# Kernel optimization log

Measured on AMD Instinct MI355X. Metric: run time of the kernel, lower is better.

Reference implementation:

```python
import jax, jax.numpy as jnp
import numpy as np

EPS = 1e-08


def setup_inputs() -> dict:
    key = jax.random.key(0)
    B, C, T = 4, 512, 32000
    x = jax.random.normal(key, (B, C, T), dtype=jnp.float32)
    weight = jnp.ones((C,), dtype=jnp.float32)
    bias = jnp.zeros((C,), dtype=jnp.float32)
    return {"x": x, "weight": weight, "bias": bias}


def reference(x, weight, bias):
    # Cumulative LayerNorm over (C, 0..t) for each time step t, 3D input (B, C, T).
    # Note: sum_C(cumsum_T(x)) == cumsum_T(sum_C(x)); reduce channels first (cheaper, same math).
    B, C, T = x.shape
    step = jnp.arange(1, T + 1, dtype=x.dtype)            # (T,)
    count = (step * C)[None, None, :]                     # (1,1,T)
    cum_sum = jnp.cumsum(x.sum(axis=1, keepdims=True), axis=-1)          # (B,1,T)
    cum_sum_sq = jnp.cumsum((x * x).sum(axis=1, keepdims=True), axis=-1)  # (B,1,T)
    cum_mean = cum_sum / count
    cum_var = jnp.maximum(cum_sum_sq / count - cum_mean * cum_mean, 0.0)
    y = (x - cum_mean) / jnp.sqrt(cum_var + EPS)
    return y * weight[None, :, None] + bias[None, :, None]
```

## Files before the change

### kernel.cpp

```cpp
#include <hip/hip_runtime.h>
#include <math.h>

#define EPS 1e-8

constexpr int CSPLIT = 4;
constexpr int CH = 1024;

__global__ __launch_bounds__(256) void clnorm_colsum(
    const float* __restrict__ x, float* __restrict__ psum,
    float* __restrict__ psumsq, int B, int C, int T) {
  int t = blockIdx.x * 256 + threadIdx.x;
  if (t >= T) return;
  int b = blockIdx.y;
  int s = blockIdx.z;
  int cPer = C / CSPLIT;
  const float* xp = x + ((size_t)b * C + (size_t)s * cPer) * (size_t)T + t;
  float sum = 0.f, sq = 0.f;
#pragma unroll 8
  for (int c = 0; c < cPer; ++c) {
    float v = xp[(size_t)c * T];
    sum += v;
    sq = fmaf(v, v, sq);
  }
  size_t o = ((size_t)s * B + b) * (size_t)T + t;
  psum[o] = sum;
  psumsq[o] = sq;
}

__global__ __launch_bounds__(256) void clnorm_chunktot(
    const float* __restrict__ psum, const float* __restrict__ psumsq,
    double* __restrict__ chunkTot, int B, int T, int nCh) {
  int ch = blockIdx.x;
  int b = blockIdx.y;
  int tid = threadIdx.x;
  int base = ch * CH;

  double ls = 0.0, lq = 0.0;
#pragma unroll
  for (int j = 0; j < CH / 256; ++j) {
    int t = base + tid + j * 256;
    if (t < T) {
      float s = 0.f, q = 0.f;
#pragma unroll
      for (int k = 0; k < CSPLIT; ++k) {
        size_t o = ((size_t)k * B + b) * (size_t)T + t;
        s += psum[o];
        q += psumsq[o];
      }
      ls += (double)s;
      lq += (double)q;
    }
  }
  __shared__ double sh_s[256];
  __shared__ double sh_q[256];
  sh_s[tid] = ls;
  sh_q[tid] = lq;
  __syncthreads();
  for (int off = 128; off > 0; off >>= 1) {
    if (tid < off) {
      sh_s[tid] += sh_s[tid + off];
      sh_q[tid] += sh_q[tid + off];
    }
    __syncthreads();
  }
  if (tid == 0) {
    chunkTot[((size_t)b * nCh + ch) * 2 + 0] = sh_s[0];
    chunkTot[((size_t)b * nCh + ch) * 2 + 1] = sh_q[0];
  }
}

__global__ __launch_bounds__(256) void clnorm_scanemit(
    const float* __restrict__ psum, const float* __restrict__ psumsq,
    const double* __restrict__ chunkTot, float* __restrict__ mean,
    float* __restrict__ rstd, int B, int C, int T, int nCh) {
  int ch = blockIdx.x;
  int b = blockIdx.y;
  int tid = threadIdx.x;
  int base = ch * CH;

  __shared__ double sv_s[CH];
  __shared__ double sv_q[CH];
  __shared__ double tp_s[256];
  __shared__ double tp_q[256];
  __shared__ double off_sq[2];

  if (tid == 0) {
    double os = 0.0, oq = 0.0;
    for (int c0 = 0; c0 < ch; ++c0) {
      os += chunkTot[((size_t)b * nCh + c0) * 2 + 0];
      oq += chunkTot[((size_t)b * nCh + c0) * 2 + 1];
    }
    off_sq[0] = os;
    off_sq[1] = oq;
  }

#pragma unroll
  for (int j = 0; j < CH / 256; ++j) {
    int idx = tid + j * 256;
    int t = base + idx;
    float s = 0.f, q = 0.f;
    if (t < T) {
#pragma unroll
      for (int k = 0; k < CSPLIT; ++k) {
        size_t o = ((size_t)k * B + b) * (size_t)T + t;
        s += psum[o];
        q += psumsq[o];
      }
    }
    sv_s[idx] = (double)s;
    sv_q[idx] = (double)q;
  }
  __syncthreads();

  const int E = CH / 256;
  double ts = 0.0, tq = 0.0;
#pragma unroll
  for (int j = 0; j < E; ++j) {
    ts += sv_s[tid * E + j];
    tq += sv_q[tid * E + j];
  }
  tp_s[tid] = ts;
  tp_q[tid] = tq;
  __syncthreads();
  for (int off = 1; off < 256; off <<= 1) {
    double vs = (tid >= off) ? tp_s[tid - off] : 0.0;
    double vq = (tid >= off) ? tp_q[tid - off] : 0.0;
    __syncthreads();
    tp_s[tid] += vs;
    tp_q[tid] += vq;
    __syncthreads();
  }
  double run_s = off_sq[0] + tp_s[tid] - ts;
  double run_q = off_sq[1] + tp_q[tid] - tq;

  int idx0 = tid * E;
  int t0 = base + idx0;
  float m_out[E], r_out[E];
#pragma unroll
  for (int j = 0; j < E; ++j) {
    run_s += sv_s[idx0 + j];
    run_q += sv_q[idx0 + j];
    double cnt = (double)(t0 + j + 1) * (double)C;
    double m = run_s / cnt;
    double var = run_q / cnt - m * m;
    if (var < 0.0) var = 0.0;
    m_out[j] = (float)m;
    r_out[j] = (float)(1.0 / sqrt(var + EPS));
  }
  size_t mo = (size_t)b * T + t0;
  if (t0 + E <= T) {
    *(float4*)(mean + mo) = make_float4(m_out[0], m_out[1], m_out[2], m_out[3]);
    *(float4*)(rstd + mo) = make_float4(r_out[0], r_out[1], r_out[2], r_out[3]);
  } else {
    for (int j = 0; j < E; ++j)
      if (t0 + j < T) {
        mean[mo + j] = m_out[j];
        rstd[mo + j] = r_out[j];
      }
  }
}

__global__ __launch_bounds__(256) void clnorm_apply(
    const float4* __restrict__ x4, const float* __restrict__ w,
    const float* __restrict__ bias, const float4* __restrict__ mean4,
    const float4* __restrict__ rstd4, float4* __restrict__ y4,
    int B, int C, int T4) {
  int t4 = blockIdx.x * 256 + threadIdx.x;
  if (t4 >= T4) return;
  int c = blockIdx.y;
  int b = blockIdx.z;
  size_t id = ((size_t)b * C + c) * (size_t)T4 + t4;
  size_t mo = (size_t)b * T4 + t4;
  float4 xv = x4[id];
  float4 mv = mean4[mo];
  float4 rv = rstd4[mo];
  float wc = w[c];
  float bc = bias[c];
  float4 yv;
  yv.x = (xv.x - mv.x) * rv.x * wc + bc;
  yv.y = (xv.y - mv.y) * rv.y * wc + bc;
  yv.z = (xv.z - mv.z) * rv.z * wc + bc;
  yv.w = (xv.w - mv.w) * rv.w * wc + bc;
  y4[id] = yv;
}

extern "C" void kernel_launch(void* const* d_in, const int* in_sizes, int n_in,
                              void* d_out, int out_size, void* d_ws,
                              size_t ws_size, hipStream_t stream) {
  const float* x = (const float*)d_in[0];
  const float* w = (const float*)d_in[1];
  const float* bias = (const float*)d_in[2];
  float* out = (float*)d_out;

  const int B = 4;
  int C = in_sizes[1];
  int T = in_sizes[0] / (B * C);
  int nCh = (T + CH - 1) / CH;

  float* ws = (float*)d_ws;
  size_t pn = (size_t)CSPLIT * B * T;
  float* psum = ws;
  float* psumsq = psum + pn;
  float* mean = psumsq + pn;
  float* rstd = mean + (size_t)B * T;
  double* chunkTot = (double*)(rstd + (size_t)B * T);

  dim3 g1((T + 255) / 256, B, CSPLIT);
  clnorm_colsum<<<g1, 256, 0, stream>>>(x, psum, psumsq, B, C, T);

  dim3 g2(nCh, B);
  clnorm_chunktot<<<g2, 256, 0, stream>>>(psum, psumsq, chunkTot, B, T, nCh);
  clnorm_scanemit<<<g2, 256, 0, stream>>>(psum, psumsq, chunkTot, mean, rstd,
                                          B, C, T, nCh);

  int T4 = T / 4;
  dim3 g3((T4 + 255) / 256, C, B);
  clnorm_apply<<<g3, 256, 0, stream>>>((const float4*)x, w, bias,
                                       (const float4*)mean,
                                       (const float4*)rstd, (float4*)out, B, C,
                                       T4);
}
```

Measured before the change: 492.0 us.

## Process batches sequentially so x slice stays in cache between passes

Result: slower. 529.9 us (+7.7%).

```diff
diff --git a/kernel.cpp b/kernel.cpp
--- a/kernel.cpp
+++ b/kernel.cpp
@@ -3,52 +3,50 @@
 
 #define EPS 1e-8
 
-constexpr int CSPLIT = 4;
+constexpr int CSPLIT = 16;
 constexpr int CH = 1024;
 
-__global__ __launch_bounds__(256) void clnorm_colsum(
-    const float* __restrict__ x, float* __restrict__ psum,
-    float* __restrict__ psumsq, int B, int C, int T) {
-  int t = blockIdx.x * 256 + threadIdx.x;
-  if (t >= T) return;
-  int b = blockIdx.y;
-  int s = blockIdx.z;
+__global__ __launch_bounds__(256) void clnorm_colsum_b(
+    const float4* __restrict__ x4, float4* __restrict__ psum4,
+    float4* __restrict__ psumsq4, int b, int C, int T4) {
+  int t4 = blockIdx.x * 256 + threadIdx.x;
+  if (t4 >= T4) return;
+  int s = blockIdx.y;
   int cPer = C / CSPLIT;
-  const float* xp = x + ((size_t)b * C + (size_t)s * cPer) * (size_t)T + t;
-  float sum = 0.f, sq = 0.f;
+  const float4* xp = x4 + ((size_t)b * C + (size_t)s * cPer) * (size_t)T4 + t4;
+  float4 sum = make_float4(0.f, 0.f, 0.f, 0.f);
+  float4 sq = make_float4(0.f, 0.f, 0.f, 0.f);
 #pragma unroll 8
   for (int c = 0; c < cPer; ++c) {
-    float v = xp[(size_t)c * T];
-    sum += v;
-    sq = fmaf(v, v, sq);
-  }
-  size_t o = ((size_t)s * B + b) * (size_t)T + t;
-  psum[o] = sum;
-  psumsq[o] = sq;
-}
-
-__global__ __launch_bounds__(256) void clnorm_chunktot(
-    const float* __restrict__ psum, const float* __restrict__ psumsq,
-    double* __restrict__ chunkTot, int B, int T, int nCh) {
+    float4 v = xp[(size_t)c * T4];
+    sum.x += v.x;
+    sum.y += v.y;
+    sum.z += v.z;
+    sum.w += v.w;
+    sq.x = fmaf(v.x, v.x, sq.x);
+    sq.y = fmaf(v.y, v.y, sq.y);
+    sq.z = fmaf(v.z, v.z, sq.z);
+    sq.w = fmaf(v.w, v.w, sq.w);
+  }
+  size_t o = (size_t)s * T4 + t4;
+  psum4[o] = sum;
+  psumsq4[o] = sq;
+}
+
+__global__ __launch_bounds__(256) void clnorm_chunktot_b(
+    const float4* __restrict__ psum4, const float4* __restrict__ psumsq4,
+    double* __restrict__ chunkTot, int T4) {
   int ch = blockIdx.x;
-  int b = blockIdx.y;
   int tid = threadIdx.x;
-  int base = ch * CH;
-
+  int t4 = ch * 256 + tid;
   double ls = 0.0, lq = 0.0;
+  if (t4 < T4) {
 #pragma unroll
-  for (int j = 0; j < CH / 256; ++j) {
-    int t = base + tid + j * 256;
-    if (t < T) {
-      float s = 0.f, q = 0.f;
-#pragma unroll
-      for (int k = 0; k < CSPLIT; ++k) {
-        size_t o = ((size_t)k * B + b) * (size_t)T + t;
-        s += psum[o];
-        q += psumsq[o];
-      }
-      ls += (double)s;
-      lq += (double)q;
+    for (int k = 0; k < CSPLIT; ++k) {
+      float4 s4 = psum4[(size_t)k * T4 + t4];
+      float4 q4 = psumsq4[(size_t)k * T4 + t4];
+      ls += (double)((s4.x + s4.y) + (s4.z + s4.w));
+      lq += (double)((q4.x + q4.y) + (q4.z + q4.w));
     }
   }
   __shared__ double sh_s[256];
@@ -64,22 +62,20 @@
     __syncthreads();
   }
   if (tid == 0) {
-    chunkTot[((size_t)b * nCh + ch) * 2 + 0] = sh_s[0];
-    chunkTot[((size_t)b * nCh + ch) * 2 + 1] = sh_q[0];
-  }
-}
-
-__global__ __launch_bounds__(256) void clnorm_scanemit(
-    const float* __restrict__ psum, const float* __restrict__ psumsq,
+    chunkTot[(size_t)ch * 2 + 0] = sh_s[0];
+    chunkTot[(size_t)ch * 2 + 1] = sh_q[0];
+  }
+}
+
+__global__ __launch_bounds__(256) void clnorm_scanemit_b(
+    const float4* __restrict__ psum4, const float4* __restrict__ psumsq4,
     const double* __restrict__ chunkTot, float* __restrict__ mean,
-    float* __restrict__ rstd, int B, int C, int T, int nCh) {
+    float* __restrict__ rstd, int b, int C, int T, int nCh) {
   int ch = blockIdx.x;
-  int b = blockIdx.y;
   int tid = threadIdx.x;
-  int base = ch * CH;
-
-  __shared__ double sv_s[CH];
-  __shared__ double sv_q[CH];
+  int T4 = T / 4;
+  int t4 = ch * 256 + tid;
+
   __shared__ double tp_s[256];
   __shared__ double tp_q[256];
   __shared__ double off_sq[2];
@@ -87,38 +83,32 @@
   if (tid == 0) {
     double os = 0.0, oq = 0.0;
     for (int c0 = 0; c0 < ch; ++c0) {
-      os += chunkTot[((size_t)b * nCh + c0) * 2 + 0];
-      oq += chunkTot[((size_t)b * nCh + c0) * 2 + 1];
+      os += chunkTot[(size_t)c0 * 2 + 0];
+      oq += chunkTot[(size_t)c0 * 2 + 1];
     }
     off_sq[0] = os;
     off_sq[1] = oq;
   }
 
+  double ds[4] = {0.0, 0.0, 0.0, 0.0};
+  double dq[4] = {0.0, 0.0, 0.0, 0.0};
+  if (t4 < T4) {
 #pragma unroll
-  for (int j = 0; j < CH / 256; ++j) {
-    int idx = tid + j * 256;
-    int t = base + idx;
-    float s = 0.f, q = 0.f;
-    if (t < T) {
-#pragma unroll
-      for (int k = 0; k < CSPLIT; ++k) {
-        size_t o = ((size_t)k * B + b) * (size_t)T + t;
-        s += psum[o];
-        q += psumsq[o];
-      }
-    }
-    sv_s[idx] = (double)s;
-    sv_q[idx] = (double)q;
-  }
-  __syncthreads();
-
-  const int E = CH / 256;
-  double ts = 0.0, tq = 0.0;
-#pragma unroll
-  for (int j = 0; j < E; ++j) {
-    ts += sv_s[tid * E + j];
-    tq += sv_q[tid * E + j];
-  }
+    for (int k = 0; k < CSPLIT; ++k) {
+      float4 s4 = psum4[(size_t)k * T4 + t4];
+      float4 q4 = psumsq4[(size_t)k * T4 + t4];
+      ds[0] += (double)s4.x;
+      ds[1] += (double)s4.y;
+      ds[2] += (double)s4.z;
+      ds[3] += (double)s4.w;
+      dq[0] += (double)q4.x;
+      dq[1] += (double)q4.y;
+      dq[2] += (double)q4.z;
+      dq[3] += (double)q4.w;
+    }
+  }
+  double ts = (ds[0] + ds[1]) + (ds[2] + ds[3]);
+  double tq = (dq[0] + dq[1]) + (dq[2] + dq[3]);
   tp_s[tid] = ts;
   tp_q[tid] = tq;
   __syncthreads();
@@ -133,13 +123,12 @@
   double run_s = off_sq[0] + tp_s[tid] - ts;
   double run_q = off_sq[1] + tp_q[tid] - tq;
 
-  int idx0 = tid * E;
-  int t0 = base + idx0;
-  float m_out[E], r_out[E];
+  int t0 = t4 * 4;
+  float m_out[4], r_out[4];
 #pragma unroll
-  for (int j = 0; j < E; ++j) {
-    run_s += sv_s[idx0 + j];
-    run_q += sv_q[idx0 + j];
+  for (int j = 0; j < 4; ++j) {
+    run_s += ds[j];
+    run_q += dq[j];
     double cnt = (double)(t0 + j + 1) * (double)C;
     double m = run_s / cnt;
     double var = run_q / cnt - m * m;
@@ -147,28 +136,21 @@
     m_out[j] = (float)m;
     r_out[j] = (float)(1.0 / sqrt(var + EPS));
   }
-  size_t mo = (size_t)b * T + t0;
-  if (t0 + E <= T) {
+  if (t0 < T) {
+    size_t mo = (size_t)b * T + t0;
     *(float4*)(mean + mo) = make_float4(m_out[0], m_out[1], m_out[2], m_out[3]);
     *(float4*)(rstd + mo) = make_float4(r_out[0], r_out[1], r_out[2], r_out[3]);
-  } else {
-    for (int j = 0; j < E; ++j)
-      if (t0 + j < T) {
-        mean[mo + j] = m_out[j];
-        rstd[mo + j] = r_out[j];
-      }
-  }
-}
-
-__global__ __launch_bounds__(256) void clnorm_apply(
+  }
+}
+
+__global__ __launch_bounds__(256) void clnorm_apply_b(
     const float4* __restrict__ x4, const float* __restrict__ w,
     const float* __restrict__ bias, const float4* __restrict__ mean4,
     const float4* __restrict__ rstd4, float4* __restrict__ y4,
-    int B, int C, int T4) {
+    int b, int C, int T4) {
   int t4 = blockIdx.x * 256 + threadIdx.x;
   if (t4 >= T4) return;
   int c = blockIdx.y;
-  int b = blockIdx.z;
   size_t id = ((size_t)b * C + c) * (size_t)T4 + t4;
   size_t mo = (size_t)b * T4 + t4;
   float4 xv = x4[id];
@@ -195,28 +177,33 @@
   const int B = 4;
   int C = in_sizes[1];
   int T = in_sizes[0] / (B * C);
+  int T4 = T / 4;
   int nCh = (T + CH - 1) / CH;
 
   float* ws = (float*)d_ws;
-  size_t pn = (size_t)CSPLIT * B * T;
+  size_t pn = (size_t)CSPLIT * T;
   float* psum = ws;
   float* psumsq = psum + pn;
   float* mean = psumsq + pn;
   float* rstd = mean + (size_t)B * T;
   double* chunkTot = (double*)(rstd + (size_t)B * T);
 
-  dim3 g1((T + 255) / 256, B, CSPLIT);
-  clnorm_colsum<<<g1, 256, 0, stream>>>(x, psum, psumsq, B, C, T);
-
-  dim3 g2(nCh, B);
-  clnorm_chunktot<<<g2, 256, 0, stream>>>(psum, psumsq, chunkTot, B, T, nCh);
-  clnorm_scanemit<<<g2, 256, 0, stream>>>(psum, psumsq, chunkTot, mean, rstd,
-                                          B, C, T, nCh);
-
-  int T4 = T / 4;
-  dim3 g3((T4 + 255) / 256, C, B);
-  clnorm_apply<<<g3, 256, 0, stream>>>((const float4*)x, w, bias,
-                                       (const float4*)mean,
-                                       (const float4*)rstd, (float4*)out, B, C,
-                                       T4);
-}
+  dim3 gc((T4 + 255) / 256, CSPLIT);
+  dim3 g2(nCh);
+  dim3 ga((T4 + 255) / 256, C);
+
+  for (int b = 0; b < B; ++b) {
+    clnorm_colsum_b<<<gc, 256, 0, stream>>>((const float4*)x, (float4*)psum,
+                                            (float4*)psumsq, b, C, T4);
+    clnorm_chunktot_b<<<g2, 256, 0, stream>>>((const float4*)psum,
+                                              (const float4*)psumsq, chunkTot,
+                                              T4);
+    clnorm_scanemit_b<<<g2, 256, 0, stream>>>((const float4*)psum,
+                                              (const float4*)psumsq, chunkTot,
+                                              mean, rstd, b, C, T, nCh);
+    clnorm_apply_b<<<ga, 256, 0, stream>>>((const float4*)x, w, bias,
+                                           (const float4*)mean,
+                                           (const float4*)rstd, (float4*)out,
+                                           b, C, T4);
+  }
+}
```
